# Optimization experiments

Hardware: AMD Instinct MI355X
Metric: run time of the kernel (lower is better)

## Reference

```python
import jax, jax.numpy as jnp
import numpy as np

IN_SZ = 256
OUT_SZ = 256
RANK = 60  # min(60, IN_SZ*OUT_SZ)
C = 512    # channel_size
N_SEL = 256
B = 1024


def setup_inputs() -> dict:
    key = jax.random.key(0)
    k_x, k_u, k_v, k_b, k_i = jax.random.split(key, 5)
    # match torch init scales: U ~ U(-sqrt(3/rank), ...), V ~ U(-sqrt(1/(in*out)),...)
    bu = np.sqrt(3.0 / RANK)
    bv = np.sqrt(1.0 / (IN_SZ * OUT_SZ))
    bb = np.sqrt(1.0 / RANK)
    x = jax.random.normal(k_x, (N_SEL, B, IN_SZ), dtype=jnp.float32)
    weights_U = jax.random.uniform(k_u, (C, RANK), jnp.float32, -bu, bu)
    weights_V = jax.random.uniform(k_v, (RANK, IN_SZ * OUT_SZ), jnp.float32, -bv, bv)
    bias = jax.random.uniform(k_b, (C, 1, OUT_SZ), jnp.float32, -bb, bb)
    indices = jax.random.randint(k_i, (N_SEL,), 0, C, dtype=jnp.int64)
    return {"x": x, "indices": indices, "weights_U": weights_U,
            "weights_V": weights_V, "bias": bias}


def reference(x, indices, weights_U, weights_V, bias):
    # Synthesize full per-channel weights, then gather selected channels
    # (faithful to the original: full U @ V materialized before gather).
    weight = (weights_U @ weights_V).reshape(-1, IN_SZ, OUT_SZ)  # [C, in, out]
    w = weight[indices]                                          # [n, in, out]
    # per-channel batched matmul: [n, B, in] x [n, in, out] -> [n, B, out]
    out = jnp.einsum('nbi,nio->nbo', x, w) + bias[indices]
    return out
```

## Files before the change

### kernel.cpp

```cpp
#include <hip/hip_runtime.h>
#include <hip/hip_bf16.h>
#include <stdint.h>

#define IN_SZ   256
#define OUT_SZ  256
#define RANK    60
#define NSEL    256
#define BATCH   1024
#define WELEMS  (IN_SZ * OUT_SZ)

typedef __attribute__((ext_vector_type(8))) short          short8;
typedef __attribute__((ext_vector_type(4))) float          f32x4;

static __device__ __forceinline__ unsigned short f32_to_bf16(float f) {
    union { float f; uint32_t u; } c; c.f = f;
    uint32_t u = c.u;
    u += 0x7fffu + ((u >> 16) & 1u);
    return (unsigned short)(u >> 16);
}

static __device__ __forceinline__ short8 cvt8(f32x4 lo, f32x4 hi) {
    union { short8 s; __hip_bfloat162 h[4]; } u;
    u.h[0] = __float22bfloat162_rn(make_float2(lo[0], lo[1]));
    u.h[1] = __float22bfloat162_rn(make_float2(lo[2], lo[3]));
    u.h[2] = __float22bfloat162_rn(make_float2(hi[0], hi[1]));
    u.h[3] = __float22bfloat162_rn(make_float2(hi[2], hi[3]));
    return u.s;
}

__global__ __launch_bounds__(256) void synth_w(
    const float* __restrict__ U, const float* __restrict__ V,
    const int* __restrict__ idx, unsigned short* __restrict__ wt)
{
    __shared__ unsigned short Cs[16][2064];

    int bid = blockIdx.x;
    int L   = (bid & 7) * 64 + (bid >> 3);
    int ic  = L >> 4;
    int g16 = L & 15;

    int tid = threadIdx.x, lane = tid & 63, wv = tid >> 6;

    int arow = lane & 15;
    int c    = idx[g16 * 16 + arow];
    short8 afr[2];
    #pragma unroll
    for (int ks = 0; ks < 2; ++ks) {
        short8 h;
        #pragma unroll
        for (int j = 0; j < 8; ++j) {
            int r = ks * 32 + (lane >> 4) * 8 + j;
            float u = (r < RANK) ? U[c * RANK + r] : 0.f;
            h[j] = (short)f32_to_bf16(u);
        }
        afr[ks] = h;
    }

    const float* Vb = V + (size_t)ic * 2048;
    #pragma unroll 2
    for (int mt = 0; mt < 32; ++mt) {
        int mloc = (wv * 32 + mt) * 16 + (lane & 15);
        f32x4 acc = {};
        #pragma unroll
        for (int ks = 0; ks < 2; ++ks) {
            short8 b;
            #pragma unroll
            for (int j = 0; j < 8; ++j) {
                int r = ks * 32 + (lane >> 4) * 8 + j;
                float v = (r < RANK) ? Vb[(size_t)r * WELEMS + mloc] : 0.f;
                b[j] = (short)f32_to_bf16(v);
            }
            acc = __builtin_amdgcn_mfma_f32_16x16x32_bf16(afr[ks], b, acc, 0, 0, 0);
        }
        #pragma unroll
        for (int j = 0; j < 4; ++j) {
            int nl = (lane >> 4) * 4 + j;
            Cs[nl][wv * 512 + mt * 16 + (lane & 15)] = f32_to_bf16(acc[j]);
        }
    }
    __syncthreads();

    #pragma unroll
    for (int t0 = 0; t0 < 16; ++t0) {
        int t  = t0 * 256 + tid;
        int nl = t >> 8;
        int o  = t & 255;
        short8 h;
        #pragma unroll
        for (int il = 0; il < 8; ++il) h[il] = (short)Cs[nl][il * 256 + o];
        int n = g16 * 16 + nl;
        size_t base = (size_t)n * WELEMS + (size_t)ic * 2048 + (size_t)o * 8;
        *reinterpret_cast<short8*>(wt + base) = h;
    }
}

__global__ __launch_bounds__(256, 2) void gemm_k(
    const float* __restrict__ x, const int* __restrict__ idx,
    const unsigned short* __restrict__ wt, const float* __restrict__ bias,
    float* __restrict__ out)
{
    __shared__ __align__(16) unsigned short As[64 * 256];

    int bid = blockIdx.x;
    int L   = (bid & 7) * 512 + (bid >> 3);
    int n   = L >> 4;
    int mt  = L & 15;

    int tid  = threadIdx.x;
    int lane = tid & 63;
    int wv   = tid >> 6;
    int r16  = lane & 15;
    int q    = lane >> 4;

    const float*          xn = x  + (size_t)n * (BATCH * IN_SZ) + (size_t)mt * 64 * IN_SZ;
    const unsigned short* wq = wt + (size_t)n * WELEMS + q * 2048
                                  + (size_t)(wv * 64 + r16) * 8;

    auto loadB = [&](int ks, short8* dst) {
        #pragma unroll
        for (int nf = 0; nf < 4; ++nf)
            dst[nf] = *reinterpret_cast<const short8*>(
                wq + (size_t)ks * 8192 + nf * 128);
    };

    f32x4  acc[4][4] = {};
    short8 bf[4][4];

    #pragma unroll
    for (int p = 0; p < 8; ++p) {
        int id    = p * 256 + tid;
        int row   = id >> 5;
        int chunk = id & 31;
        const float* gp = xn + (size_t)row * IN_SZ + chunk * 8;
        f32x4 v0 = __builtin_nontemporal_load(reinterpret_cast<const f32x4*>(gp));
        f32x4 v1 = __builtin_nontemporal_load(reinterpret_cast<const f32x4*>(gp) + 1);
        int off = row * 512 + ((chunk * 16) ^ ((row & 7) << 4));
        *reinterpret_cast<short8*>(&As[off >> 1]) = cvt8(v0, v1);
    }
    loadB(0, bf[0]);
    loadB(1, bf[1]);
    loadB(2, bf[2]);
    __syncthreads();

    #pragma unroll
    for (int ks = 0; ks < 8; ++ks) {
        if (ks < 5) loadB(ks + 3, bf[(ks + 3) % 4]);
        short8 af[4];
        #pragma unroll
        for (int mf = 0; mf < 4; ++mf) {
            int row = mf * 16 + r16;
            int off = row * 512 + ((ks * 64 + q * 16) ^ ((row & 7) << 4));
            af[mf] = *reinterpret_cast<const short8*>(&As[off >> 1]);
        }
        const short8* bb = bf[ks % 4];
        #pragma unroll
        for (int mf = 0; mf < 4; ++mf)
            #pragma unroll
            for (int nf = 0; nf < 4; ++nf)
                acc[mf][nf] = __builtin_amdgcn_mfma_f32_16x16x32_bf16(
                    bb[nf], af[mf], acc[mf][nf], 0, 0, 0);
    }

    int c = idx[n];
    float* on = out + (size_t)n * (BATCH * OUT_SZ) + (size_t)mt * 64 * OUT_SZ;
    #pragma unroll
    for (int nf = 0; nf < 4; ++nf) {
        f32x4 bv = *reinterpret_cast<const f32x4*>(
            &bias[(size_t)c * OUT_SZ + wv * 64 + nf * 16 + q * 4]);
        #pragma unroll
        for (int mf = 0; mf < 4; ++mf) {
            f32x4 w = acc[mf][nf] + bv;
            __builtin_nontemporal_store(w, reinterpret_cast<f32x4*>(
                &on[(size_t)(mf * 16 + r16) * OUT_SZ + wv * 64 + nf * 16 + q * 4]));
        }
    }
}

extern "C" void kernel_launch(void* const* d_in, const int* in_sizes, int n_in,
                              void* d_out, int out_size, void* d_ws, size_t ws_size,
                              hipStream_t stream) {
    const float* x    = (const float*)d_in[0];
    const int*   idx  = (const int*)  d_in[1];
    const float* U    = (const float*)d_in[2];
    const float* V    = (const float*)d_in[3];
    const float* bias = (const float*)d_in[4];
    float* out = (float*)d_out;
    unsigned short* wt = (unsigned short*)d_ws;
    (void)in_sizes; (void)n_in; (void)out_size; (void)ws_size;

    synth_w<<<dim3(512),  dim3(256), 0, stream>>>(U, V, idx, wt);
    gemm_k <<<dim3(4096), dim3(256), 0, stream>>>(x, idx, wt, bias, out);
}
```

Baseline: 180.3 us.

## Stage full per-channel weight in LDS and stream x rows through registers

The GEMM kernel now launches one 512-thread block per selected channel instead of 16 blocks per channel. Each block copies that channel's whole bf16 weight matrix (128KB) into LDS using direct global-to-LDS loads, which removes the 16-fold re-reading of weights from L2. Each wave then walks 128 batch rows in 16-row steps, prefetching the next x tile into registers as a double buffer and starting the accumulators from the bias held in LDS. The trade-off is one block and 8 waves per CU with heavy LDS and register use, no overlap between the weight load and compute, and plain stores where nontemporal stores were used before.

```diff
diff --git a/kernel.cpp b/kernel.cpp
--- a/kernel.cpp
+++ b/kernel.cpp
@@ -94,85 +94,85 @@
     }
 }
 
-__global__ __launch_bounds__(256, 2) void gemm_k(
+__global__ __launch_bounds__(512, 2) void gemm_k(
     const float* __restrict__ x, const int* __restrict__ idx,
     const unsigned short* __restrict__ wt, const float* __restrict__ bias,
     float* __restrict__ out)
 {
-    __shared__ __align__(16) unsigned short As[64 * 256];
+    __shared__ __align__(16) unsigned short Wl[WELEMS];
+    __shared__ __align__(16) float          Bl[256];
 
-    int bid = blockIdx.x;
-    int L   = (bid & 7) * 512 + (bid >> 3);
-    int n   = L >> 4;
-    int mt  = L & 15;
-
+    int n    = blockIdx.x;
     int tid  = threadIdx.x;
     int lane = tid & 63;
     int wv   = tid >> 6;
     int r16  = lane & 15;
     int q    = lane >> 4;
 
-    const float*          xn = x  + (size_t)n * (BATCH * IN_SZ) + (size_t)mt * 64 * IN_SZ;
-    const unsigned short* wq = wt + (size_t)n * WELEMS + q * 2048
-                                  + (size_t)(wv * 64 + r16) * 8;
+    const unsigned short* wn = wt + (size_t)n * WELEMS;
 
-    auto loadB = [&](int ks, short8* dst) {
+    #pragma unroll
+    for (int j = 0; j < 16; ++j) {
+        int g = wv * 16 + j;
+        __builtin_amdgcn_global_load_lds(
+            (const __attribute__((address_space(1))) void*)(wn + g * 512 + lane * 8),
+            (__attribute__((address_space(3))) void*)(&Wl[g * 512]),
+            16, 0, 0);
+    }
+    int c = idx[n];
+    if (tid < 64) {
+        f32x4 b = *reinterpret_cast<const f32x4*>(bias + (size_t)c * OUT_SZ + tid * 4);
+        *reinterpret_cast<f32x4*>(&Bl[tid * 4]) = b;
+    }
+    __syncthreads();
+
+    const float* xw = x + (size_t)n * (BATCH * IN_SZ)
+                        + (size_t)(wv * 128 + r16) * IN_SZ + q * 8;
+    float*       ow = out + (size_t)n * (BATCH * OUT_SZ)
+                        + (size_t)(wv * 128 + r16) * OUT_SZ + q * 4;
+    const char*  wl = reinterpret_cast<const char*>(Wl);
+    int lq = q * 4096 + r16 * 16;
+
+    f32x4 A0[8][2], A1[8][2];
+
+    auto loadA = [&](f32x4 (&Ab)[8][2], int t) {
+        const float* xp = xw + (size_t)t * 16 * IN_SZ;
         #pragma unroll
-        for (int nf = 0; nf < 4; ++nf)
-            dst[nf] = *reinterpret_cast<const short8*>(
-                wq + (size_t)ks * 8192 + nf * 128);
+        for (int ks = 0; ks < 8; ++ks) {
+            Ab[ks][0] = *reinterpret_cast<const f32x4*>(xp + ks * 32);
+            Ab[ks][1] = *reinterpret_cast<const f32x4*>(xp + ks * 32 + 4);
+        }
     };
 
-    f32x4  acc[4][4] = {};
-    short8 bf[4][4];
+    loadA(A0, 0);
 
     #pragma unroll
-    for (int p = 0; p < 8; ++p) {
-        int id    = p * 256 + tid;
-        int row   = id >> 5;
-        int chunk = id & 31;
-        const float* gp = xn + (size_t)row * IN_SZ + chunk * 8;
-        f32x4 v0 = __builtin_nontemporal_load(reinterpret_cast<const f32x4*>(gp));
-        f32x4 v1 = __builtin_nontemporal_load(reinterpret_cast<const f32x4*>(gp) + 1);
-        int off = row * 512 + ((chunk * 16) ^ ((row & 7) << 4));
-        *reinterpret_cast<short8*>(&As[off >> 1]) = cvt8(v0, v1);
-    }
-    loadB(0, bf[0]);
-    loadB(1, bf[1]);
-    loadB(2, bf[2]);
-    __syncthreads();
+    for (int t = 0; t < 8; ++t) {
+        f32x4 (&Ac)[8][2] = (t & 1) ? A1 : A0;
+        f32x4 (&An)[8][2] = (t & 1) ? A0 : A1;
+        if (t < 7) loadA(An, t + 1);
 
-    #pragma unroll
-    for (int ks = 0; ks < 8; ++ks) {
-        if (ks < 5) loadB(ks + 3, bf[(ks + 3) % 4]);
-        short8 af[4];
+        f32x4 acc[16];
         #pragma unroll
-        for (int mf = 0; mf < 4; ++mf) {
-            int row = mf * 16 + r16;
-            int off = row * 512 + ((ks * 64 + q * 16) ^ ((row & 7) << 4));
-            af[mf] = *reinterpret_cast<const short8*>(&As[off >> 1]);
+        for (int nf = 0; nf < 16; ++nf)
+            acc[nf] = *reinterpret_cast<const f32x4*>(&Bl[nf * 16 + q * 4]);
+
+        #pragma unroll
+        for (int ks = 0; ks < 8; ++ks) {
+            short8 af = cvt8(Ac[ks][0], Ac[ks][1]);
+            #pragma unroll
+            for (int nf = 0; nf < 16; ++nf) {
+                short8 bf = *reinterpret_cast<const short8*>(
+                    wl + lq + ks * 16384 + nf * 256);
+                acc[nf] = __builtin_amdgcn_mfma_f32_16x16x32_bf16(
+                    bf, af, acc[nf], 0, 0, 0);
+            }
         }
-        const short8* bb = bf[ks % 4];
+
+        float* op = ow + (size_t)t * 16 * OUT_SZ;
         #pragma unroll
-        for (int mf = 0; mf < 4; ++mf)
-            #pragma unroll
-            for (int nf = 0; nf < 4; ++nf)
-                acc[mf][nf] = __builtin_amdgcn_mfma_f32_16x16x32_bf16(
-                    bb[nf], af[mf], acc[mf][nf], 0, 0, 0);
-    }
-
-    int c = idx[n];
-    float* on = out + (size_t)n * (BATCH * OUT_SZ) + (size_t)mt * 64 * OUT_SZ;
-    #pragma unroll
-    for (int nf = 0; nf < 4; ++nf) {
-        f32x4 bv = *reinterpret_cast<const f32x4*>(
-            &bias[(size_t)c * OUT_SZ + wv * 64 + nf * 16 + q * 4]);
-        #pragma unroll
-        for (int mf = 0; mf < 4; ++mf) {
-            f32x4 w = acc[mf][nf] + bv;
-            __builtin_nontemporal_store(w, reinterpret_cast<f32x4*>(
-                &on[(size_t)(mf * 16 + r16) * OUT_SZ + wv * 64 + nf * 16 + q * 4]));
-        }
+        for (int nf = 0; nf < 16; ++nf)
+            *reinterpret_cast<f32x4*>(op + nf * 16) = acc[nf];
     }
 }
 
@@ -188,6 +188,6 @@
     unsigned short* wt = (unsigned short*)d_ws;
     (void)in_sizes; (void)n_in; (void)out_size; (void)ws_size;
 
-    synth_w<<<dim3(512),  dim3(256), 0, stream>>>(U, V, idx, wt);
-    gemm_k <<<dim3(4096), dim3(256), 0, stream>>>(x, idx, wt, bias, out);
+    synth_w<<<dim3(512), dim3(256), 0, stream>>>(U, V, idx, wt);
+    gemm_k <<<dim3(256), dim3(512), 0, stream>>>(x, idx, wt, bias, out);
 }
```

New measurement: 190.5 us. +5.6%, slower.
